# Optimization experiments

Hardware: AMD Instinct MI355X
Metric: run time of the kernel (lower is better)

Reference implementation:

```python
import jax, jax.numpy as jnp
import numpy as np

N_USERS = 200000
N_ITEMS = 50000
N_ENTITIES = 150000
N_RELATIONS = 32
N_EDGES = 2000000
N_INTER = 1000000
N_HOPS = 2
D = 64


def setup_inputs() -> dict:
    key = jax.random.key(0)
    ks = jax.random.split(key, 10)
    return {
        "user_emb": jax.random.normal(ks[0], (N_USERS, D), jnp.float32) * 0.1,
        "entity_emb": jax.random.normal(ks[1], (N_ENTITIES, D), jnp.float32) * 0.1,
        "weight": jax.random.normal(ks[2], (N_RELATIONS, D), jnp.float32) * 0.1,
        "g1_w": jax.random.normal(ks[3], (D, D), jnp.float32) * 0.1,
        "g2_w": jax.random.normal(ks[4], (D, D), jnp.float32) * 0.1,
        "edge_head": jax.random.randint(ks[5], (N_EDGES,), 0, N_ENTITIES),
        "edge_tail": jax.random.randint(ks[6], (N_EDGES,), 0, N_ENTITIES),
        "edge_type": jax.random.randint(ks[7], (N_EDGES,), 0, N_RELATIONS),
        "mat_row": jax.random.randint(ks[8], (N_INTER,), 0, N_USERS),
        "mat_col": jax.random.randint(ks[9], (N_INTER,), 0, N_ITEMS),
    }


def _scatter_mean(src, index, num_segments):
    s = jax.ops.segment_sum(src, index, num_segments=num_segments)
    cnt = jax.ops.segment_sum(jnp.ones((src.shape[0],), src.dtype), index,
                              num_segments=num_segments)
    return s / jnp.maximum(cnt, 1.0)[:, None]


def _l2norm(x, eps=1e-12):
    n = jnp.sqrt(jnp.sum(x * x, axis=-1, keepdims=True))
    return x / jnp.maximum(n, eps)


def reference(user_emb, entity_emb, weight, g1_w, g2_w,
              edge_head, edge_tail, edge_type, mat_row, mat_col):
    entity_res = entity_emb
    user_res = user_emb
    item_kg_res = jnp.zeros((N_ITEMS, D), entity_emb.dtype)
    item_int_res = jnp.zeros((N_ITEMS, D), entity_emb.dtype)

    for _ in range(N_HOPS):
        # KG aggregation: gather tail embs, modulate by relation emb, scatter-mean to head
        neigh = entity_emb[edge_tail] * weight[edge_type]            # [E, D]
        entity_agg = _scatter_mean(neigh, edge_head, N_ENTITIES)      # [n_ent, D]
        item_kg_agg = entity_agg[:N_ITEMS]
        att_kg_agg = entity_agg[N_ITEMS:]
        # interaction aggregation: mean of user embs per item
        item_int_agg = _scatter_mean(user_emb[mat_row], mat_col, N_ITEMS)
        # gated fusion (F.linear: x @ W.T)
        gi = jax.nn.sigmoid(item_kg_agg @ g1_w.T + item_int_agg @ g2_w.T)
        item_fusion = gi * item_kg_agg + (1.0 - gi) * item_int_agg
        # user_agg = sparse.mm(user_item, item_fusion) == segment-sum over rows
        user_agg = jax.ops.segment_sum(item_fusion[mat_col], mat_row,
                                       num_segments=N_USERS)
        entity_emb = _l2norm(jnp.concatenate([item_fusion, att_kg_agg], axis=0))
        user_emb = _l2norm(user_agg)
        item_kg_n = _l2norm(item_kg_agg)
        item_int_n = _l2norm(item_int_agg)
        entity_res = entity_res + entity_emb
        user_res = user_res + user_emb
        item_kg_res = item_kg_res + item_kg_n
        item_int_res = item_int_res + item_int_n

    return (entity_res, user_res, item_kg_res, item_int_res)
```

## Files before the change

### kernel.cpp

```cpp
#include <hip/hip_runtime.h>
#include <math.h>

#define N_USERS    200000
#define N_ITEMS    50000
#define N_ENTITIES 150000
#define N_EDGES    2000000
#define N_INTER    1000000
#define D          64

#define CHUNK      1250
#define THR_OWN    5
#define NBLK_E     120
#define NBLK_C     40
#define NBLK_R     160
#define NBLK_TOT   (NBLK_E + NBLK_C + NBLK_R)

#define RK     16384
#define NS     16
#define NR_E   10
#define NR_C   4
#define NR_R   13
#define NR_TOT (NR_E + NR_C + NR_R)
#define KTOT   (N_ENTITIES + N_ITEMS + N_USERS)

#define EB     2048
#define IB     1024

#define FT    64
#define FPAD  132
#define NTILE ((N_ITEMS + FT - 1) / FT)

__device__ __forceinline__ unsigned short f2bf(float f) {
    unsigned u = __float_as_uint(f);
    u += 0x7FFFu + ((u >> 16) & 1u);
    return (unsigned short)(u >> 16);
}
__device__ __forceinline__ ushort4 f2bf4(float4 f) {
    ushort4 o;
    o.x = f2bf(f.x); o.y = f2bf(f.y); o.z = f2bf(f.z); o.w = f2bf(f.w);
    return o;
}
__device__ __forceinline__ float4 bf2f4(ushort4 h) {
    float4 f;
    f.x = __uint_as_float(((unsigned)h.x) << 16);
    f.y = __uint_as_float(((unsigned)h.y) << 16);
    f.z = __uint_as_float(((unsigned)h.z) << 16);
    f.w = __uint_as_float(((unsigned)h.w) << 16);
    return f;
}

__device__ __forceinline__ float qsum16(float v) {
#pragma unroll
    for (int off = 1; off < 16; off <<= 1) v += __shfl_xor(v, off, 64);
    return v;
}

__global__ void prep_k(const float4* __restrict__ a, ushort4* __restrict__ ab, int na4,
                       const float4* __restrict__ b, ushort4* __restrict__ bb, int nb4,
                       const int* __restrict__ tail, const int* __restrict__ type,
                       int* __restrict__ packed) {
    int n = na4 + nb4 + N_EDGES;
    for (int i = blockIdx.x * blockDim.x + threadIdx.x; i < n;
         i += gridDim.x * blockDim.x) {
        if (i < na4) ab[i] = f2bf4(a[i]);
        else if (i < na4 + nb4) bb[i - na4] = f2bf4(b[i - na4]);
        else {
            int j = i - na4 - nb4;
            packed[j] = tail[j] | (type[j] << 18);
        }
    }
}

__device__ __forceinline__ void range_geom(int r, const int*& src, int& n,
                                           int& base, int& cbase, int& rlen,
                                           const int* head, const int* mcol,
                                           const int* mrow) {
    if (r < NR_E) {
        src = head; n = N_EDGES; base = r * RK; cbase = 0;
        rlen = N_ENTITIES - base;
    } else if (r < NR_E + NR_C) {
        src = mcol; n = N_INTER; base = (r - NR_E) * RK;
        cbase = N_ENTITIES; rlen = N_ITEMS - base;
    } else {
        src = mrow; n = N_INTER; base = (r - NR_E - NR_C) * RK;
        cbase = N_ENTITIES + N_ITEMS; rlen = N_USERS - base;
    }
    if (rlen > RK) rlen = RK;
}

__global__ void hist_part_k(const int* __restrict__ head,
                            const int* __restrict__ mcol,
                            const int* __restrict__ mrow,
                            int* __restrict__ partial) {
    __shared__ int lh[RK];
    int r = blockIdx.x >> 4, s = blockIdx.x & (NS - 1);
    for (int d = threadIdx.x; d < RK; d += 256) lh[d] = 0;
    __syncthreads();
    const int* src; int n, base, cbase, rlen;
    range_geom(r, src, n, base, cbase, rlen, head, mcol, mrow);
    int chunk = n / NS;
    int lo = s * chunk, hi = lo + chunk;
    int i = lo + threadIdx.x;
    for (; i + 768 < hi; i += 1024) {
        unsigned d0 = (unsigned)(__builtin_nontemporal_load(&src[i])       - base);
        unsigned d1 = (unsigned)(__builtin_nontemporal_load(&src[i + 256]) - base);
        unsigned d2 = (unsigned)(__builtin_nontemporal_load(&src[i + 512]) - base);
        unsigned d3 = (unsigned)(__builtin_nontemporal_load(&src[i + 768]) - base);
        if (d0 < (unsigned)RK) atomicAdd(&lh[d0], 1);
        if (d1 < (unsigned)RK) atomicAdd(&lh[d1], 1);
        if (d2 < (unsigned)RK) atomicAdd(&lh[d2], 1);
        if (d3 < (unsigned)RK) atomicAdd(&lh[d3], 1);
    }
    for (; i < hi; i += 256) {
        unsigned d = (unsigned)(__builtin_nontemporal_load(&src[i]) - base);
        if (d < (unsigned)RK) atomicAdd(&lh[d], 1);
    }
    __syncthreads();
    int* dst = partial + (size_t)s * KTOT + cbase + base;
    for (int d = threadIdx.x; d < rlen; d += 256) dst[d] = lh[d];
}

__global__ void scanA_k(const int* __restrict__ partial,
                        int* __restrict__ blk_sums) {
    __shared__ int ss[256];
    int b = blockIdx.x, t = threadIdx.x;
    int base = b * CHUNK;
    int sum = 0;
    if (t < 250) {
        int g = base + t * THR_OWN;
#pragma unroll
        for (int s = 0; s < NS; ++s) {
            const int* p = partial + (size_t)s * KTOT + g;
#pragma unroll
            for (int j = 0; j < THR_OWN; ++j) sum += p[j];
        }
    }
    ss[t] = sum;
    __syncthreads();
    for (int off = 128; off > 0; off >>= 1) {
        if (t < off) ss[t] += ss[t + off];
        __syncthreads();
    }
    if (t == 0) blk_sums[b] = ss[0];
}

__global__ void scanB_k(int* __restrict__ blk_sums, int* __restrict__ blk_off,
                        int* __restrict__ e_starts, int* __restrict__ c_starts,
                        int* __restrict__ r_starts) {
    __shared__ int ss[512];
    int t = threadIdx.x;
    ss[t] = (t < NBLK_TOT) ? blk_sums[t] : 0;
    __syncthreads();
    for (int off = 1; off < 512; off <<= 1) {
        int v = (t >= off) ? ss[t - off] : 0;
        __syncthreads();
        ss[t] += v;
        __syncthreads();
    }
    if (t < NBLK_TOT) {
        int excl = (t == 0) ? 0 : ss[t - 1];
        int segstart_excl;
        if (t < NBLK_E) segstart_excl = 0;
        else if (t < NBLK_E + NBLK_C) segstart_excl = ss[NBLK_E - 1];
        else segstart_excl = ss[NBLK_E + NBLK_C - 1];
        blk_off[t] = excl - segstart_excl;
    }
    if (t == 0) {
        e_starts[N_ENTITIES] = N_EDGES;
        c_starts[N_ITEMS]    = N_INTER;
        r_starts[N_USERS]    = N_INTER;
    }
}

__global__ void scanC_k(const int* __restrict__ partial,
                        const int* __restrict__ blk_off,
                        int* __restrict__ e_starts, int* __restrict__ c_starts,
                        int* __restrict__ r_starts,
                        int* __restrict__ e_curs, int* __restrict__ c_curs,
                        int* __restrict__ r_curs) {
    __shared__ int ss[256];
    int b = blockIdx.x, t = threadIdx.x;
    int base = b * CHUNK;
    int tot[THR_OWN];
    int sum = 0;
    if (t < 250) {
        int g = base + t * THR_OWN;
#pragma unroll
        for (int j = 0; j < THR_OWN; ++j) tot[j] = 0;
#pragma unroll
        for (int s = 0; s < NS; ++s) {
            const int* p = partial + (size_t)s * KTOT + g;
#pragma unroll
            for (int j = 0; j < THR_OWN; ++j) tot[j] += p[j];
        }
#pragma unroll
        for (int j = 0; j < THR_OWN; ++j) sum += tot[j];
    }
    ss[t] = sum;
    __syncthreads();
    for (int off = 1; off < 256; off <<= 1) {
        int v = (t >= off) ? ss[t - off] : 0;
        __syncthreads();
        ss[t] += v;
        __syncthreads();
    }
    if (t < 250) {
        int run = blk_off[b] + ((t == 0) ? 0 : ss[t - 1]);
        int* sarr; int* carr; int ebase;
        if (b < NBLK_E)               { sarr = e_starts; carr = e_curs; ebase = base; }
        else if (b < NBLK_E + NBLK_C) { sarr = c_starts; carr = c_curs; ebase = base - NBLK_E * CHUNK; }
        else                          { sarr = r_starts; carr = r_curs; ebase = base - (NBLK_E + NBLK_C) * CHUNK; }
        int gl = ebase + t * THR_OWN;
#pragma unroll
        for (int j = 0; j < THR_OWN; ++j) {
            sarr[gl + j] = run;
            carr[gl + j] = run;
            run += tot[j];
        }
    }
}

__global__ void permute_e_k(const int* __restrict__ head,
                            const int* __restrict__ packed,
                            int* __restrict__ ec, int* __restrict__ e_sorted) {
    int xcd = blockIdx.x & 7;
    int slot = blockIdx.x >> 3;
    int nslot = gridDim.x >> 3;
    int lo = xcd * (N_ENTITIES / 8);
    int hi = lo + (N_ENTITIES / 8);
    for (int i = slot * blockDim.x + threadIdx.x; i < N_EDGES;
         i += nslot * blockDim.x) {
        int h = __builtin_nontemporal_load(&head[i]);
        if (h >= lo && h < hi) {
            int pos = atomicAdd(&ec[h], 1);
            e_sorted[pos] = __builtin_nontemporal_load(&packed[i]);
        }
    }
}

__global__ void permute_i_k(const int* __restrict__ mcol, const int* __restrict__ mrow,
                            int* __restrict__ cc, int* __restrict__ rc,
                            int* __restrict__ i_srow, int* __restrict__ i_scol) {
    int xcd = blockIdx.x & 7;
    int slot = blockIdx.x >> 3;
    int nslot = gridDim.x >> 3;
    int clo = xcd * (N_ITEMS / 8), chi = clo + (N_ITEMS / 8);
    int rlo = xcd * (N_USERS / 8), rhi = rlo + (N_USERS / 8);
    for (int i = slot * blockDim.x + threadIdx.x; i < N_INTER;
         i += nslot * blockDim.x) {
        int c = __builtin_nontemporal_load(&mcol[i]);
        int r = __builtin_nontemporal_load(&mrow[i]);
        if (c >= clo && c < chi) {
            int pos = atomicAdd(&cc[c], 1);
            i_srow[pos] = r;
        }
        if (r >= rlo && r < rhi) {
            int pos = atomicAdd(&rc[r], 1);
            i_scol[pos] = c;
        }
    }
}

__global__ void agg_all_k(const ushort4* __restrict__ ent_bf,
                          const float* __restrict__ ent0f,
                          const float* __restrict__ wrel,
                          const int* __restrict__ es,
                          const int* __restrict__ e_sorted,
                          float* __restrict__ agg,
                          ushort4* __restrict__ ent_cur_bf,
                          float* __restrict__ ent_res,
                          const ushort4* __restrict__ usr_bf,
                          const int* __restrict__ cs,
                          const int* __restrict__ i_srow,
                          float* __restrict__ iint,
                          int first) {
    int lane = threadIdx.x & 63;
    int q = lane >> 4, ql = lane & 15;
    int qb = lane & 48;
    if (blockIdx.x < EB) {
        __shared__ float4 wl4[32 * 16];
        for (int idx = threadIdx.x; idx < 512; idx += 256)
            wl4[idx] = ((const float4*)wrel)[idx];
        __syncthreads();
        int qid = (blockIdx.x * 4 + (threadIdx.x >> 6)) * 4 + q;
        int nq = EB * 16;
        for (int h = qid; h < N_ENTITIES; h += nq) {
            int beg = es[h], end = es[h + 1];
            float4 a0 = {0, 0, 0, 0}, a1 = {0, 0, 0, 0};
            for (int j0 = beg; j0 < end; j0 += 16) {
                int p = (j0 + ql < end) ? e_sorted[j0 + ql] : 0;
                int mm = end - j0; if (mm > 16) mm = 16;
                int k = 0;
                for (; k + 1 < mm; k += 2) {
                    int p0 = __shfl(p, qb | k, 64);
                    int p1 = __shfl(p, qb | (k + 1), 64);
                    float4 e0 = bf2f4(ent_bf[(size_t)(p0 & 0x3FFFF) * 16 + ql]);
                    float4 w0 = wl4[((p0 >> 18) << 4) + ql];
                    float4 e1 = bf2f4(ent_bf[(size_t)(p1 & 0x3FFFF) * 16 + ql]);
                    float4 w1 = wl4[((p1 >> 18) << 4) + ql];
                    a0.x = fmaf(e0.x, w0.x, a0.x); a0.y = fmaf(e0.y, w0.y, a0.y);
                    a0.z = fmaf(e0.z, w0.z, a0.z); a0.w = fmaf(e0.w, w0.w, a0.w);
                    a1.x = fmaf(e1.x, w1.x, a1.x); a1.y = fmaf(e1.y, w1.y, a1.y);
                    a1.z = fmaf(e1.z, w1.z, a1.z); a1.w = fmaf(e1.w, w1.w, a1.w);
                }
                if (k < mm) {
                    int p0 = __shfl(p, qb | k, 64);
                    float4 e0 = bf2f4(ent_bf[(size_t)(p0 & 0x3FFFF) * 16 + ql]);
                    float4 w0 = wl4[((p0 >> 18) << 4) + ql];
                    a0.x = fmaf(e0.x, w0.x, a0.x); a0.y = fmaf(e0.y, w0.y, a0.y);
                    a0.z = fmaf(e0.z, w0.z, a0.z); a0.w = fmaf(e0.w, w0.w, a0.w);
                }
            }
            float4 v; v.x = a0.x + a1.x; v.y = a0.y + a1.y;
            v.z = a0.z + a1.z; v.w = a0.w + a1.w;
            if (h < N_ITEMS) {
                int d = end - beg;
                float inv = 1.0f / (float)(d > 0 ? d : 1);
                float4 o; o.x = v.x * inv; o.y = v.y * inv;
                o.z = v.z * inv; o.w = v.w * inv;
                ((float4*)agg)[(size_t)h * 16 + ql] = o;
            } else {
                float s = qsum16(fmaf(v.x, v.x, fmaf(v.y, v.y, fmaf(v.z, v.z, v.w * v.w))));
                float inv = 1.0f / fmaxf(sqrtf(s), 1e-12f);
                float4 vn; vn.x = v.x * inv; vn.y = v.y * inv;
                vn.z = v.z * inv; vn.w = v.w * inv;
                size_t o4 = (size_t)h * 16 + ql;
                if (first) {
                    ent_cur_bf[o4] = f2bf4(vn);
                    float4 b = ((const float4*)ent0f)[o4];
                    b.x += vn.x; b.y += vn.y; b.z += vn.z; b.w += vn.w;
                    ((float4*)ent_res)[o4] = b;
                } else {
                    float4 r = ((float4*)ent_res)[o4];
                    r.x += vn.x; r.y += vn.y; r.z += vn.z; r.w += vn.w;
                    ((float4*)ent_res)[o4] = r;
                }
            }
        }
    } else {
        int qid = ((blockIdx.x - EB) * 4 + (threadIdx.x >> 6)) * 4 + q;
        int nq = IB * 16;
        for (int c = qid; c < N_ITEMS; c += nq) {
            int beg = cs[c], end = cs[c + 1];
            float4 a0 = {0, 0, 0, 0}, a1 = {0, 0, 0, 0};
            for (int j0 = beg; j0 < end; j0 += 16) {
                int p = (j0 + ql < end) ? i_srow[j0 + ql] : 0;
                int mm = end - j0; if (mm > 16) mm = 16;
                int k = 0;
                for (; k + 1 < mm; k += 2) {
                    int p0 = __shfl(p, qb | k, 64);
                    int p1 = __shfl(p, qb | (k + 1), 64);
                    float4 u0 = bf2f4(usr_bf[(size_t)p0 * 16 + ql]);
                    float4 u1 = bf2f4(usr_bf[(size_t)p1 * 16 + ql]);
                    a0.x += u0.x; a0.y += u0.y; a0.z += u0.z; a0.w += u0.w;
                    a1.x += u1.x; a1.y += u1.y; a1.z += u1.z; a1.w += u1.w;
                }
                if (k < mm) {
                    int p0 = __shfl(p, qb | k, 64);
                    float4 u0 = bf2f4(usr_bf[(size_t)p0 * 16 + ql]);
                    a0.x += u0.x; a0.y += u0.y; a0.z += u0.z; a0.w += u0.w;
                }
            }
            float4 v; v.x = a0.x + a1.x; v.y = a0.y + a1.y;
            v.z = a0.z + a1.z; v.w = a0.w + a1.w;
            int d = end - beg;
            float inv = 1.0f / (float)(d > 0 ? d : 1);
            float4 o; o.x = v.x * inv; o.y = v.y * inv;
            o.z = v.z * inv; o.w = v.w * inv;
            ((float4*)iint)[(size_t)c * 16 + ql] = o;
        }
    }
}

__global__ void fuse_k(const float* __restrict__ agg,
                       const float* __restrict__ iint,
                       const float* __restrict__ g1,
                       const float* __restrict__ g2,
                       const float* __restrict__ ent0,
                       unsigned short* __restrict__ ifus_bf,
                       unsigned short* __restrict__ ent_cur_bf,
                       float* __restrict__ ent_res,
                       float* __restrict__ kg_res,
                       float* __restrict__ int_res,
                       int first) {
    __shared__ float A[FT * FPAD];
    __shared__ float B[64 * FPAD];
    int t = threadIdx.x;
    int ibase = blockIdx.x * FT;

    {
        const float4* g14 = (const float4*)g1;
        const float4* g24 = (const float4*)g2;
        const float4* a4 = (const float4*)(agg + (size_t)ibase * D);
        const float4* i4 = (const float4*)(iint + (size_t)ibase * D);
        for (int idx = t; idx < 1024; idx += 256) {
            int r = idx >> 4, kq = idx & 15;
            ((float4*)&B[r * FPAD])[kq]      = g14[idx];
            ((float4*)&B[r * FPAD + 64])[kq] = g24[idx];
            ((float4*)&A[r * FPAD])[kq]      = a4[idx];
            ((float4*)&A[r * FPAD + 64])[kq] = i4[idx];
        }
    }
    __syncthreads();

    int ti = t >> 4, tj = t & 15;

    float y[4][4] = {};
    for (int k = 0; k < 128; k += 4) {
        float4 av[4], bv[4];
#pragma unroll
        for (int a = 0; a < 4; ++a) av[a] = *(const float4*)&A[(ti + 16 * a) * FPAD + k];
#pragma unroll
        for (int b = 0; b < 4; ++b) bv[b] = *(const float4*)&B[(tj + 16 * b) * FPAD + k];
#pragma unroll
        for (int a = 0; a < 4; ++a)
#pragma unroll
            for (int b = 0; b < 4; ++b) {
                y[a][b] = fmaf(av[a].x, bv[b].x, y[a][b]);
                y[a][b] = fmaf(av[a].y, bv[b].y, y[a][b]);
                y[a][b] = fmaf(av[a].z, bv[b].z, y[a][b]);
                y[a][b] = fmaf(av[a].w, bv[b].w, y[a][b]);
            }
    }

    float fus[4][4], kg[4][4], ii[4][4];
    float sf[4], sk[4], si[4];
#pragma unroll
    for (int a = 0; a < 4; ++a) { sf[a] = 0.f; sk[a] = 0.f; si[a] = 0.f; }
#pragma unroll
    for (int a = 0; a < 4; ++a) {
        int i = ti + 16 * a;
#pragma unroll
        for (int b = 0; b < 4; ++b) {
            int j = tj + 16 * b;
            float K = A[i * FPAD + j];
            float I = A[i * FPAD + 64 + j];
            float gi = 1.0f / (1.0f + __expf(-y[a][b]));
            float f = gi * K + (1.0f - gi) * I;
            fus[a][b] = f; kg[a][b] = K; ii[a][b] = I;
            sf[a] = fmaf(f, f, sf[a]);
            sk[a] = fmaf(K, K, sk[a]);
            si[a] = fmaf(I, I, si[a]);
        }
    }
#pragma unroll
    for (int off = 1; off < 16; off <<= 1) {
#pragma unroll
        for (int a = 0; a < 4; ++a) {
            sf[a] += __shfl_xor(sf[a], off, 64);
            sk[a] += __shfl_xor(sk[a], off, 64);
            si[a] += __shfl_xor(si[a], off, 64);
        }
    }

#pragma unroll
    for (int a = 0; a < 4; ++a) {
        int i = ibase + ti + 16 * a;
        if (i < N_ITEMS) {
            float nf = 1.0f / fmaxf(sqrtf(sf[a]), 1e-12f);
            float nk = 1.0f / fmaxf(sqrtf(sk[a]), 1e-12f);
            float ni = 1.0f / fmaxf(sqrtf(si[a]), 1e-12f);
#pragma unroll
            for (int b = 0; b < 4; ++b) {
                size_t o = (size_t)i * D + tj + 16 * b;
                float f = fus[a][b];
                ifus_bf[o] = f2bf(f);
                float fn = f * nf;
                ent_cur_bf[o] = f2bf(fn);
                if (first) {
                    ent_res[o] = ent0[o] + fn;
                    kg_res[o]  = kg[a][b] * nk;
                    int_res[o] = ii[a][b] * ni;
                } else {
                    ent_res[o] += fn;
                    kg_res[o]  += kg[a][b] * nk;
                    int_res[o] += ii[a][b] * ni;
                }
            }
        }
    }
}

__global__ void user_agg_k(const ushort4* __restrict__ ifus_bf,
                           const int* __restrict__ rs,
                           const int* __restrict__ i_scol,
                           const float* __restrict__ usr0,
                           ushort4* __restrict__ usr_cur_bf,
                           float* __restrict__ usr_res,
                           int first) {
    const float4* u04 = (const float4*)usr0;
    int lane = threadIdx.x & 63;
    int q = lane >> 4, ql = lane & 15;
    int qb = lane & 48;
    int qid = (blockIdx.x * (blockDim.x >> 6) + (threadIdx.x >> 6)) * 4 + q;
    int nq = gridDim.x * (blockDim.x >> 6) * 4;
    for (int u = qid; u < N_USERS; u += nq) {
        int beg = rs[u], end = rs[u + 1];
        float4 a0 = {0, 0, 0, 0}, a1 = {0, 0, 0, 0};
        for (int j0 = beg; j0 < end; j0 += 16) {
            int p = (j0 + ql < end) ? i_scol[j0 + ql] : 0;
            int mm = end - j0; if (mm > 16) mm = 16;
            int k = 0;
            for (; k + 1 < mm; k += 2) {
                int p0 = __shfl(p, qb | k, 64);
                int p1 = __shfl(p, qb | (k + 1), 64);
                float4 u0 = bf2f4(ifus_bf[(size_t)p0 * 16 + ql]);
                float4 u1 = bf2f4(ifus_bf[(size_t)p1 * 16 + ql]);
                a0.x += u0.x; a0.y += u0.y; a0.z += u0.z; a0.w += u0.w;
                a1.x += u1.x; a1.y += u1.y; a1.z += u1.z; a1.w += u1.w;
            }
            if (k < mm) {
                int p0 = __shfl(p, qb | k, 64);
                float4 u0 = bf2f4(ifus_bf[(size_t)p0 * 16 + ql]);
                a0.x += u0.x; a0.y += u0.y; a0.z += u0.z; a0.w += u0.w;
            }
        }
        float4 v; v.x = a0.x + a1.x; v.y = a0.y + a1.y;
        v.z = a0.z + a1.z; v.w = a0.w + a1.w;
        float s = qsum16(fmaf(v.x, v.x, fmaf(v.y, v.y, fmaf(v.z, v.z, v.w * v.w))));
        float inv = 1.0f / fmaxf(sqrtf(s), 1e-12f);
        float4 vn; vn.x = v.x * inv; vn.y = v.y * inv;
        vn.z = v.z * inv; vn.w = v.w * inv;
        size_t o4 = (size_t)u * 16 + ql;
        usr_cur_bf[o4] = f2bf4(vn);
        if (first) {
            float4 b = u04[o4];
            b.x += vn.x; b.y += vn.y; b.z += vn.z; b.w += vn.w;
            ((float4*)usr_res)[o4] = b;
        } else {
            float4 r = ((float4*)usr_res)[o4];
            r.x += vn.x; r.y += vn.y; r.z += vn.z; r.w += vn.w;
            ((float4*)usr_res)[o4] = r;
        }
    }
}

extern "C" void kernel_launch(void* const* d_in, const int* in_sizes, int n_in,
                              void* d_out, int out_size, void* d_ws, size_t ws_size,
                              hipStream_t stream) {
    const float* user_emb   = (const float*)d_in[0];
    const float* entity_emb = (const float*)d_in[1];
    const float* wrel       = (const float*)d_in[2];
    const float* g1         = (const float*)d_in[3];
    const float* g2         = (const float*)d_in[4];
    const int*   edge_head  = (const int*)d_in[5];
    const int*   edge_tail  = (const int*)d_in[6];
    const int*   edge_type  = (const int*)d_in[7];
    const int*   mat_row    = (const int*)d_in[8];
    const int*   mat_col    = (const int*)d_in[9];

    const size_t ENT_SZ = (size_t)N_ENTITIES * D;
    const size_t USR_SZ = (size_t)N_USERS * D;
    const size_t ITM_SZ = (size_t)N_ITEMS * D;

    float* out     = (float*)d_out;
    float* ent_res = out;
    float* usr_res = out + ENT_SZ;
    float* kg_res  = out + ENT_SZ + USR_SZ;
    float* int_res = out + ENT_SZ + USR_SZ + ITM_SZ;

    char* p = (char*)d_ws;
    unsigned short* ent_cur_bf = (unsigned short*)p; p += ENT_SZ * 2;
    unsigned short* usr_cur_bf = (unsigned short*)p; p += USR_SZ * 2;
    unsigned short* ent0_bf    = (unsigned short*)p; p += ENT_SZ * 2;
    unsigned short* usr0_bf    = (unsigned short*)p; p += USR_SZ * 2;
    float* agg  = (float*)p; p += ITM_SZ * 4;
    float* iint = (float*)p; p += ITM_SZ * 4;
    unsigned short* ifus_bf = (unsigned short*)p; p += ITM_SZ * 2;
    int* e_starts = (int*)p; p += (N_ENTITIES + 1) * 4;
    int* c_starts = (int*)p; p += (N_ITEMS + 1) * 4;
    int* r_starts = (int*)p; p += (N_USERS + 1) * 4;
    int* e_curs   = (int*)p; p += N_ENTITIES * 4;
    int* c_curs   = (int*)p; p += N_ITEMS * 4;
    int* r_curs   = (int*)p; p += N_USERS * 4;
    p = (char*)(((size_t)p + 15) & ~(size_t)15);
    int* e_sorted = (int*)p; p += (size_t)N_EDGES * 4;
    int* i_srow   = (int*)p; p += (size_t)N_INTER * 4;
    int* i_scol   = (int*)p; p += (size_t)N_INTER * 4;
    int* packed   = (int*)p; p += (size_t)N_EDGES * 4;
    int* blk_sums = (int*)p; p += NBLK_TOT * 4;
    int* blk_off  = (int*)p; p += NBLK_TOT * 4;
    int* partial = (int*)agg;

    prep_k<<<2048, 256, 0, stream>>>((const float4*)entity_emb, (ushort4*)ent0_bf,
                                     (int)(ENT_SZ / 4),
                                     (const float4*)user_emb, (ushort4*)usr0_bf,
                                     (int)(USR_SZ / 4),
                                     edge_tail, edge_type, packed);

    hist_part_k<<<NR_TOT * NS, 256, 0, stream>>>(edge_head, mat_col, mat_row, partial);
    scanA_k<<<NBLK_TOT, 256, 0, stream>>>(partial, blk_sums);
    scanB_k<<<1, 512, 0, stream>>>(blk_sums, blk_off, e_starts, c_starts, r_starts);
    scanC_k<<<NBLK_TOT, 256, 0, stream>>>(partial, blk_off,
                                          e_starts, c_starts, r_starts,
                                          e_curs, c_curs, r_curs);
    permute_e_k<<<4096, 256, 0, stream>>>(edge_head, packed, e_curs, e_sorted);
    permute_i_k<<<4096, 256, 0, stream>>>(mat_col, mat_row,
                                          c_curs, r_curs, i_srow, i_scol);

    for (int hop = 0; hop < 2; ++hop) {
        const unsigned short* ent_src = (hop == 0) ? ent0_bf : ent_cur_bf;
        const unsigned short* usr_src = (hop == 0) ? usr0_bf : usr_cur_bf;
        int first = (hop == 0);
        agg_all_k<<<EB + IB, 256, 0, stream>>>((const ushort4*)ent_src, entity_emb,
                                               wrel, e_starts, e_sorted,
                                               agg, (ushort4*)ent_cur_bf, ent_res,
                                               (const ushort4*)usr_src, c_starts,
                                               i_srow, iint, first);
        fuse_k<<<NTILE, 256, 0, stream>>>(agg, iint, g1, g2, entity_emb,
                                          ifus_bf, ent_cur_bf,
                                          ent_res, kg_res, int_res, first);
        user_agg_k<<<2048, 256, 0, stream>>>((const ushort4*)ifus_bf, r_starts,
                                             i_scol, user_emb,
                                             (ushort4*)usr_cur_bf, usr_res, first);
    }
}
```

Baseline: 604.3 us.

## Replace atomic-cursor permutation with rank-based counting-sort scatter

The histogram kernel now records each element's local rank (the return value of the shared atomic) into 16-bit rank arrays. The scan converts per-slice partial counts into exclusive offsets in place, so the permute kernels compute destinations as offset plus rank without global atomics. This removes contended global atomicAdd cursors in exchange for extra rank writes and reads and a serial per-slice offset loop in the scan kernel.

```diff
diff --git a/kernel.cpp b/kernel.cpp
--- a/kernel.cpp
+++ b/kernel.cpp
@@ -91,13 +91,18 @@
 __global__ void hist_part_k(const int* __restrict__ head,
                             const int* __restrict__ mcol,
                             const int* __restrict__ mrow,
-                            int* __restrict__ partial) {
+                            int* __restrict__ partial,
+                            unsigned short* __restrict__ rank_e,
+                            unsigned short* __restrict__ rank_c,
+                            unsigned short* __restrict__ rank_r) {
     __shared__ int lh[RK];
     int r = blockIdx.x >> 4, s = blockIdx.x & (NS - 1);
     for (int d = threadIdx.x; d < RK; d += 256) lh[d] = 0;
     __syncthreads();
     const int* src; int n, base, cbase, rlen;
     range_geom(r, src, n, base, cbase, rlen, head, mcol, mrow);
+    unsigned short* rank = (r < NR_E) ? rank_e
+                         : (r < NR_E + NR_C) ? rank_c : rank_r;
     int chunk = n / NS;
     int lo = s * chunk, hi = lo + chunk;
     int i = lo + threadIdx.x;
@@ -106,14 +111,14 @@
         unsigned d1 = (unsigned)(__builtin_nontemporal_load(&src[i + 256]) - base);
         unsigned d2 = (unsigned)(__builtin_nontemporal_load(&src[i + 512]) - base);
         unsigned d3 = (unsigned)(__builtin_nontemporal_load(&src[i + 768]) - base);
-        if (d0 < (unsigned)RK) atomicAdd(&lh[d0], 1);
-        if (d1 < (unsigned)RK) atomicAdd(&lh[d1], 1);
-        if (d2 < (unsigned)RK) atomicAdd(&lh[d2], 1);
-        if (d3 < (unsigned)RK) atomicAdd(&lh[d3], 1);
+        if (d0 < (unsigned)RK) rank[i]       = (unsigned short)atomicAdd(&lh[d0], 1);
+        if (d1 < (unsigned)RK) rank[i + 256] = (unsigned short)atomicAdd(&lh[d1], 1);
+        if (d2 < (unsigned)RK) rank[i + 512] = (unsigned short)atomicAdd(&lh[d2], 1);
+        if (d3 < (unsigned)RK) rank[i + 768] = (unsigned short)atomicAdd(&lh[d3], 1);
     }
     for (; i < hi; i += 256) {
         unsigned d = (unsigned)(__builtin_nontemporal_load(&src[i]) - base);
-        if (d < (unsigned)RK) atomicAdd(&lh[d], 1);
+        if (d < (unsigned)RK) rank[i] = (unsigned short)atomicAdd(&lh[d], 1);
     }
     __syncthreads();
     int* dst = partial + (size_t)s * KTOT + cbase + base;
@@ -172,12 +177,10 @@
     }
 }
 
-__global__ void scanC_k(const int* __restrict__ partial,
+__global__ void scanC_k(int* __restrict__ partial,
                         const int* __restrict__ blk_off,
                         int* __restrict__ e_starts, int* __restrict__ c_starts,
-                        int* __restrict__ r_starts,
-                        int* __restrict__ e_curs, int* __restrict__ c_curs,
-                        int* __restrict__ r_curs) {
+                        int* __restrict__ r_starts) {
     __shared__ int ss[256];
     int b = blockIdx.x, t = threadIdx.x;
     int base = b * CHUNK;
@@ -206,23 +209,32 @@
     }
     if (t < 250) {
         int run = blk_off[b] + ((t == 0) ? 0 : ss[t - 1]);
-        int* sarr; int* carr; int ebase;
-        if (b < NBLK_E)               { sarr = e_starts; carr = e_curs; ebase = base; }
-        else if (b < NBLK_E + NBLK_C) { sarr = c_starts; carr = c_curs; ebase = base - NBLK_E * CHUNK; }
-        else                          { sarr = r_starts; carr = r_curs; ebase = base - (NBLK_E + NBLK_C) * CHUNK; }
+        int* sarr; int ebase;
+        if (b < NBLK_E)               { sarr = e_starts; ebase = base; }
+        else if (b < NBLK_E + NBLK_C) { sarr = c_starts; ebase = base - NBLK_E * CHUNK; }
+        else                          { sarr = r_starts; ebase = base - (NBLK_E + NBLK_C) * CHUNK; }
         int gl = ebase + t * THR_OWN;
-#pragma unroll
+        int gg = base + t * THR_OWN;
         for (int j = 0; j < THR_OWN; ++j) {
             sarr[gl + j] = run;
-            carr[gl + j] = run;
-            run += tot[j];
-        }
-    }
-}
-
-__global__ void permute_e_k(const int* __restrict__ head,
+            int cur = run;
+#pragma unroll
+            for (int s = 0; s < NS; ++s) {
+                int idx = s * KTOT + gg + j;
+                int v = partial[idx];
+                partial[idx] = cur;
+                cur += v;
+            }
+            run = cur;
+        }
+    }
+}
+
+__global__ void scatter_e_k(const int* __restrict__ head,
                             const int* __restrict__ packed,
-                            int* __restrict__ ec, int* __restrict__ e_sorted) {
+                            const unsigned short* __restrict__ rank_e,
+                            const int* __restrict__ partial,
+                            int* __restrict__ e_sorted) {
     int xcd = blockIdx.x & 7;
     int slot = blockIdx.x >> 3;
     int nslot = gridDim.x >> 3;
@@ -232,14 +244,19 @@
          i += nslot * blockDim.x) {
         int h = __builtin_nontemporal_load(&head[i]);
         if (h >= lo && h < hi) {
-            int pos = atomicAdd(&ec[h], 1);
+            int s = i / (N_EDGES / NS);
+            int pos = partial[(size_t)s * KTOT + h]
+                    + (int)__builtin_nontemporal_load(&rank_e[i]);
             e_sorted[pos] = __builtin_nontemporal_load(&packed[i]);
         }
     }
 }
 
-__global__ void permute_i_k(const int* __restrict__ mcol, const int* __restrict__ mrow,
-                            int* __restrict__ cc, int* __restrict__ rc,
+__global__ void scatter_i_k(const int* __restrict__ mcol,
+                            const int* __restrict__ mrow,
+                            const unsigned short* __restrict__ rank_c,
+                            const unsigned short* __restrict__ rank_r,
+                            const int* __restrict__ partial,
                             int* __restrict__ i_srow, int* __restrict__ i_scol) {
     int xcd = blockIdx.x & 7;
     int slot = blockIdx.x >> 3;
@@ -250,12 +267,15 @@
          i += nslot * blockDim.x) {
         int c = __builtin_nontemporal_load(&mcol[i]);
         int r = __builtin_nontemporal_load(&mrow[i]);
+        int s = i / (N_INTER / NS);
         if (c >= clo && c < chi) {
-            int pos = atomicAdd(&cc[c], 1);
+            int pos = partial[(size_t)s * KTOT + N_ENTITIES + c]
+                    + (int)__builtin_nontemporal_load(&rank_c[i]);
             i_srow[pos] = r;
         }
         if (r >= rlo && r < rhi) {
-            int pos = atomicAdd(&rc[r], 1);
+            int pos = partial[(size_t)s * KTOT + N_ENTITIES + N_ITEMS + r]
+                    + (int)__builtin_nontemporal_load(&rank_r[i]);
             i_scol[pos] = c;
         }
     }
@@ -570,9 +590,9 @@
     int* e_starts = (int*)p; p += (N_ENTITIES + 1) * 4;
     int* c_starts = (int*)p; p += (N_ITEMS + 1) * 4;
     int* r_starts = (int*)p; p += (N_USERS + 1) * 4;
-    int* e_curs   = (int*)p; p += N_ENTITIES * 4;
-    int* c_curs   = (int*)p; p += N_ITEMS * 4;
-    int* r_curs   = (int*)p; p += N_USERS * 4;
+    unsigned short* rank_e = (unsigned short*)p; p += (size_t)N_EDGES * 2;
+    unsigned short* rank_c = (unsigned short*)p; p += (size_t)N_INTER * 2;
+    unsigned short* rank_r = (unsigned short*)p; p += (size_t)N_INTER * 2;
     p = (char*)(((size_t)p + 15) & ~(size_t)15);
     int* e_sorted = (int*)p; p += (size_t)N_EDGES * 4;
     int* i_srow   = (int*)p; p += (size_t)N_INTER * 4;
@@ -588,15 +608,16 @@
                                      (int)(USR_SZ / 4),
                                      edge_tail, edge_type, packed);
 
-    hist_part_k<<<NR_TOT * NS, 256, 0, stream>>>(edge_head, mat_col, mat_row, partial);
+    hist_part_k<<<NR_TOT * NS, 256, 0, stream>>>(edge_head, mat_col, mat_row,
+                                                 partial, rank_e, rank_c, rank_r);
     scanA_k<<<NBLK_TOT, 256, 0, stream>>>(partial, blk_sums);
     scanB_k<<<1, 512, 0, stream>>>(blk_sums, blk_off, e_starts, c_starts, r_starts);
     scanC_k<<<NBLK_TOT, 256, 0, stream>>>(partial, blk_off,
-                                          e_starts, c_starts, r_starts,
-                                          e_curs, c_curs, r_curs);
-    permute_e_k<<<4096, 256, 0, stream>>>(edge_head, packed, e_curs, e_sorted);
-    permute_i_k<<<4096, 256, 0, stream>>>(mat_col, mat_row,
-                                          c_curs, r_curs, i_srow, i_scol);
+                                          e_starts, c_starts, r_starts);
+    scatter_e_k<<<4096, 256, 0, stream>>>(edge_head, packed, rank_e, partial,
+                                          e_sorted);
+    scatter_i_k<<<4096, 256, 0, stream>>>(mat_col, mat_row, rank_c, rank_r,
+                                          partial, i_srow, i_scol);
 
     for (int hop = 0; hop < 2; ++hop) {
         const unsigned short* ent_src = (hop == 0) ? ent0_bf : ent_cur_bf;
```

Result: no change. 595.6 us (-1.4%).
